# Optimization experiments

Hardware: AMD Instinct MI355X
Metric: run time of the kernel (lower is better)

The kernel has to match this reference:

```python
import jax, jax.numpy as jnp
import numpy as np

BATCH, N, DIM_IN, DIM_K, DIM_V, NH = 2, 4096, 256, 256, 256, 8

def setup_inputs() -> dict:
    key = jax.random.key(0)
    k1, k2, k3, k4 = jax.random.split(key, 4)
    s = 1.0 / np.sqrt(DIM_IN)
    return {
        "x": jax.random.normal(k1, (BATCH, N, DIM_IN), dtype=jnp.float32),
        "Wq": jax.random.normal(k2, (DIM_IN, DIM_K), dtype=jnp.float32) * s,
        "Wk": jax.random.normal(k3, (DIM_IN, DIM_K), dtype=jnp.float32) * s,
        "Wv": jax.random.normal(k4, (DIM_IN, DIM_V), dtype=jnp.float32) * s,
    }

def reference(x, Wq, Wk, Wv):
    b, n, _ = x.shape
    nh = NH
    dk = DIM_K // nh
    dv = DIM_V // nh
    # project and split heads: [b, nh, n, dk]
    q = jnp.einsum('bni,ik->bnk', x, Wq).reshape(b, n, nh, dk).transpose(0, 2, 1, 3)
    k = jnp.einsum('bni,ik->bnk', x, Wk).reshape(b, n, nh, dk).transpose(0, 2, 1, 3)
    v = jnp.einsum('bni,iv->bnv', x, Wv).reshape(b, n, nh, dv).transpose(0, 2, 1, 3)
    scale = 1.0 / np.sqrt(dk)
    dist = jnp.einsum('bhqd,bhkd->bhqk', q, k) * scale  # [b, nh, n, n]
    dist = jax.nn.softmax(dist, axis=-1)
    # dropout is identity in eval mode
    att = jnp.einsum('bhqk,bhkv->bhqv', dist, v)  # [b, nh, n, dv]
    return att.transpose(0, 2, 1, 3).reshape(b, n, DIM_V)
```

## Files before the change

kernel.cpp:

```cpp
#include <hip/hip_runtime.h>
#include <math.h>

#define BATCH 2
#define SEQ   4096
#define DIN   256
#define NH    8
#define DH    32
#define BH    (BATCH*NH)
#define NSPLIT 4
#define KRANGE (SEQ/NSPLIT)
#define TILES  (KRANGE/64)
#define QTILE  256

typedef short bf16x8 __attribute__((ext_vector_type(8)));
typedef float f32x4  __attribute__((ext_vector_type(4)));

#if defined(__has_builtin)
#if __has_builtin(__builtin_amdgcn_exp2f)
#define EXP2(x) __builtin_amdgcn_exp2f(x)
#else
#define EXP2_ASM 1
#endif
#else
#define EXP2_ASM 1
#endif
#ifdef EXP2_ASM
__device__ __forceinline__ float exp2_raw(float x) {
    float r;
    asm("v_exp_f32 %0, %1\n\ts_nop 1" : "=v"(r) : "v"(x));
    return r;
}
#define EXP2(x) exp2_raw(x)
#endif

#define SC2 0.25508218f

__device__ __forceinline__ unsigned short f2bf(float f) {
    unsigned int u = __builtin_bit_cast(unsigned int, f);
    u += 0x7fffu + ((u >> 16) & 1u);
    return (unsigned short)(u >> 16);
}

__device__ __forceinline__ unsigned int pack_bf2(float f0, float f1) {
    unsigned int u0 = __builtin_bit_cast(unsigned int, f0) + 0x8000u;
    unsigned int u1 = __builtin_bit_cast(unsigned int, f1) + 0x8000u;
    return __builtin_amdgcn_perm(u1, u0, 0x07060302u);
}

__device__ __forceinline__ unsigned int pack_bf2_t(float f0, float f1) {
    return __builtin_amdgcn_perm(__builtin_bit_cast(unsigned int, f1),
                                 __builtin_bit_cast(unsigned int, f0),
                                 0x07060302u);
}

#if defined(__has_builtin)
#if __has_builtin(__builtin_amdgcn_global_load_lds)
#define HAS_ASYNC_LDS 1
#endif
#endif

__device__ __forceinline__ void stage16(const unsigned short* g,
                                        unsigned short* lds_base, int lane) {
#ifdef HAS_ASYNC_LDS
    __builtin_amdgcn_global_load_lds(
        (const __attribute__((address_space(1))) unsigned int*)g,
        (__attribute__((address_space(3))) unsigned int*)lds_base, 16, 0, 0);
#else
    *(bf16x8*)(lds_base + (size_t)lane * 8) = *(const bf16x8*)g;
#endif
}

__global__ __launch_bounds__(256) void prep_kernel(
    const float* __restrict__ Wq, const float* __restrict__ Wk, const float* __restrict__ Wv,
    unsigned short* __restrict__ Wt)
{
    __shared__ float ws[64][65];
    const int t = threadIdx.x;
    int wsel = blockIdx.x >> 4;
    int tile = blockIdx.x & 15;
    int tr = (tile >> 2) * 64;
    int tc = (tile & 3) * 64;
    const float* __restrict__ W = (wsel == 0) ? Wq : (wsel == 1) ? Wk : Wv;
    #pragma unroll
    for (int i = 0; i < 16; i++) {
        int row = i * 4 + (t >> 6), col = t & 63;
        ws[row][col] = W[(size_t)(tr + row) * DIN + tc + col];
    }
    __syncthreads();
    unsigned short* dst = Wt + (size_t)wsel * DIN * DIN;
    #pragma unroll
    for (int i = 0; i < 16; i++) {
        int orow = i * 4 + (t >> 6), ocol = t & 63;
        dst[(size_t)(tc + orow) * DIN + tr + ocol] = f2bf(ws[ocol][orow]);
    }
}

__global__ __launch_bounds__(256) void proj_kernel(
    const float* __restrict__ x, const unsigned short* __restrict__ Wt,
    unsigned short* __restrict__ qh, unsigned short* __restrict__ kh,
    unsigned short* __restrict__ vt)
{
    __shared__ __align__(16) unsigned short abuf[8][4][64][8];
    __shared__ __align__(16) unsigned short bbuf[8][4][64][8];

    const int wsel = blockIdx.y;
    const int w    = threadIdx.x >> 6;
    const int lane = threadIdx.x & 63;
    const int quad = lane >> 4;
    const int l16  = lane & 15;

    const int sl   = lane ^ (lane >> 3);
    const int sl16 = sl >> 2, squad = sl & 3;
    const int s_ = (l16 << 2) | quad;
    const int jj = (s_ & 56) | ((s_ ^ (s_ >> 3)) & 7);

    int arow0, brow0;
    const unsigned short* Wbase;
    const float* Xbase;
    unsigned short (*wdst)[4][64][8];
    unsigned short (*xdst)[4][64][8];
    if (wsel < 2) {
        int tt = blockIdx.x >> 7, nt = blockIdx.x & 127;
        arow0 = tt * 64; brow0 = nt * 64;
        Wbase = Wt + (size_t)wsel * DIN * DIN + (size_t)arow0 * DIN;
        Xbase = x + (size_t)brow0 * DIN;
        wdst = abuf; xdst = bbuf;
    } else {
        int nt = blockIdx.x >> 2, tt = blockIdx.x & 3;
        arow0 = nt * 64; brow0 = tt * 64;
        Xbase = x + (size_t)arow0 * DIN;
        Wbase = Wt + (size_t)2 * DIN * DIN + (size_t)brow0 * DIN;
        wdst = bbuf; xdst = abuf;
    }

    #pragma unroll
    for (int i = 0; i < 8; i++) {
        int id = w * 8 + i;
        int kb = id >> 2, rt = id & 3;
        stage16(Wbase + (size_t)(rt * 16 + sl16) * DIN + kb * 32 + squad * 8,
                &wdst[kb][rt][0][0], lane);
    }
    #pragma unroll
    for (int i = 0; i < 8; i++) {
        int id = w * 8 + i;
        int kb = id >> 2, rt = id & 3;
        const float4* src = (const float4*)(Xbase + (size_t)(rt * 16 + sl16) * DIN
                                            + kb * 32 + squad * 8);
        float4 a = src[0], b = src[1];
        uint4 p = { pack_bf2(a.x, a.y), pack_bf2(a.z, a.w),
                    pack_bf2(b.x, b.y), pack_bf2(b.z, b.w) };
        *(uint4*)(&xdst[kb][rt][0][0] + (size_t)lane * 8) = p;
    }
    __syncthreads();

    f32x4 acc[4];
    #pragma unroll
    for (int c = 0; c < 4; c++) acc[c] = (f32x4){0.f, 0.f, 0.f, 0.f};
    #pragma unroll
    for (int kb = 0; kb < 8; kb++) {
        bf16x8 af = *(const bf16x8*)&abuf[kb][w][jj][0];
        #pragma unroll
        for (int c = 0; c < 4; c++) {
            bf16x8 bfr = *(const bf16x8*)&bbuf[kb][c][jj][0];
            acc[c] = __builtin_amdgcn_mfma_f32_16x16x32_bf16(af, bfr, acc[c], 0, 0, 0);
        }
    }

    if (wsel < 2) {
        const float scl = (wsel == 0) ? SC2 : 1.0f;
        unsigned short* __restrict__ dst0 = (wsel == 0) ? qh : kh;
        const int t0 = arow0 + w * 16;
        const int h = t0 >> 5, d0 = (t0 & 31) + quad * 4;
        #pragma unroll
        for (int c = 0; c < 4; c++) {
            int n = brow0 + c * 16 + l16;
            int b = n >> 12, n12 = n & 4095;
            unsigned int u01 = pack_bf2(acc[c][0] * scl, acc[c][1] * scl);
            unsigned int u23 = pack_bf2(acc[c][2] * scl, acc[c][3] * scl);
            *(uint2*)&dst0[((size_t)(b * NH + h) * SEQ + n12) * DH + d0] = make_uint2(u01, u23);
        }
    } else {
        const int n0w = arow0 + w * 16;
        const int b = n0w >> 12, nbase = (n0w & 4095) + quad * 4;
        #pragma unroll
        for (int c = 0; c < 4; c++) {
            int t = brow0 + c * 16;
            int h = t >> 5, d = (t & 31) + l16;
            unsigned int u01 = pack_bf2(acc[c][0], acc[c][1]);
            unsigned int u23 = pack_bf2(acc[c][2], acc[c][3]);
            *(uint2*)&vt[((size_t)(b * NH + h) * DH + d) * SEQ + nbase] = make_uint2(u01, u23);
        }
    }
}

__global__ __launch_bounds__(256, 4) void attn_kernel(
    const unsigned short* __restrict__ qh,
    const unsigned short* __restrict__ kh,
    const unsigned short* __restrict__ vt,
    unsigned short* __restrict__ po, float* __restrict__ pl)
{
    __shared__ __align__(16) unsigned short pbuf[4][2][16][64];
    __shared__ __align__(16) unsigned short kbuf[2][4][64][8];
    __shared__ __align__(16) unsigned short vbuf[2][4][64][8];

    const int tid  = threadIdx.x;
    const int wave = tid >> 6;
    const int lane = tid & 63;
    const int quad = lane >> 4;
    const int l16  = lane & 15;
    const int sw   = l16 & 7;

    const int bh = blockIdx.x & 15;
    const int qb = (blockIdx.x >> 4) & 15;
    const int ks = blockIdx.x >> 8;
    const int q0 = qb * QTILE + wave * 64;
    const int kbase = ks * KRANGE;

    const unsigned short* __restrict__ Qp = qh + (size_t)bh * SEQ * DH;
    const unsigned short* __restrict__ Kp = kh + (size_t)bh * SEQ * DH;
    const unsigned short* __restrict__ Vp = vt + (size_t)bh * DH * SEQ;

    const int sl    = lane ^ (lane >> 3);
    const int sl16  = sl >> 2, squad = sl & 3;
    const unsigned short* ksrc = Kp + (size_t)(kbase + wave * 16 + sl16) * DH + squad * 8;
    const int vdh = wave >> 1, vkh = wave & 1;
    const unsigned short* vsrc = Vp + (size_t)(vdh * 16 + sl16) * SEQ + kbase + vkh * 32 + squad * 8;

    const int s_ = (l16 << 2) | quad;
    const int jj = (s_ & 56) | ((s_ ^ (s_ >> 3)) & 7);

    bf16x8 qf[4];
    #pragma unroll
    for (int i = 0; i < 4; i++)
        qf[i] = *(const bf16x8*)(Qp + (size_t)(q0 + i * 16 + l16) * DH + quad * 8);

    const bf16x8 ones = {0x3F80, 0x3F80, 0x3F80, 0x3F80,
                         0x3F80, 0x3F80, 0x3F80, 0x3F80};

    f32x4 o[4][2];
    f32x4 lones[4];
    #pragma unroll
    for (int i = 0; i < 4; i++) {
        o[i][0] = (f32x4){0.f, 0.f, 0.f, 0.f};
        o[i][1] = (f32x4){0.f, 0.f, 0.f, 0.f};
        lones[i] = (f32x4){0.f, 0.f, 0.f, 0.f};
    }
    const f32x4 z = {0.f, 0.f, 0.f, 0.f};

    stage16(ksrc, &kbuf[0][wave][0][0], lane);
    stage16(vsrc, &vbuf[0][wave][0][0], lane);
    ksrc += 64 * DH;
    vsrc += 64;

    for (int t = 0; t < TILES; t++) {
        const int buf = t & 1;

        __syncthreads();

        if (t + 1 < TILES) {
            stage16(ksrc, &kbuf[buf ^ 1][wave][0][0], lane);
            stage16(vsrc, &vbuf[buf ^ 1][wave][0][0], lane);
            ksrc += 64 * DH;
            vsrc += 64;
        }

        bf16x8 kf[4], vf[4];
        #pragma unroll
        for (int c = 0; c < 4; c++) kf[c] = *(const bf16x8*)&kbuf[buf][c][jj][0];
        #pragma unroll
        for (int f = 0; f < 4; f++) vf[f] = *(const bf16x8*)&vbuf[buf][f][jj][0];

        #pragma unroll
        for (int qt = 0; qt < 4; qt++) {
            const int pr = qt & 1;
            #pragma unroll
            for (int c = 0; c < 4; c++) {
                f32x4 s = __builtin_amdgcn_mfma_f32_16x16x32_bf16(kf[c], qf[qt], z, 0, 0, 0);
                float e0 = EXP2(s[0]);
                float e1 = EXP2(s[1]);
                float e2 = EXP2(s[2]);
                float e3 = EXP2(s[3]);
                int chs = ((c * 2 + (quad >> 1)) ^ sw) * 8 + (quad & 1) * 4;
                *(uint2*)&pbuf[wave][pr][l16][chs] =
                    make_uint2(pack_bf2_t(e0, e1), pack_bf2_t(e2, e3));
            }
            bf16x8 pf0 = *(const bf16x8*)&pbuf[wave][pr][l16][((0 + quad) ^ sw) * 8];
            bf16x8 pf1 = *(const bf16x8*)&pbuf[wave][pr][l16][((4 + quad) ^ sw) * 8];
            __builtin_amdgcn_s_setprio(1);
            o[qt][0] = __builtin_amdgcn_mfma_f32_16x16x32_bf16(pf0, vf[0], o[qt][0], 0, 0, 0);
            o[qt][0] = __builtin_amdgcn_mfma_f32_16x16x32_bf16(pf1, vf[1], o[qt][0], 0, 0, 0);
            o[qt][1] = __builtin_amdgcn_mfma_f32_16x16x32_bf16(pf0, vf[2], o[qt][1], 0, 0, 0);
            o[qt][1] = __builtin_amdgcn_mfma_f32_16x16x32_bf16(pf1, vf[3], o[qt][1], 0, 0, 0);
            lones[qt] = __builtin_amdgcn_mfma_f32_16x16x32_bf16(pf0, ones, lones[qt], 0, 0, 0);
            lones[qt] = __builtin_amdgcn_mfma_f32_16x16x32_bf16(pf1, ones, lones[qt], 0, 0, 0);
            __builtin_amdgcn_s_setprio(0);
        }
    }

    const size_t obase = (size_t)(ks * BH + bh) * SEQ;
    #pragma unroll
    for (int qt = 0; qt < 4; qt++) {
        if (l16 == 0) {
            #pragma unroll
            for (int r = 0; r < 4; r++)
                pl[obase + q0 + qt * 16 + quad * 4 + r] = lones[qt][r];
        }
        #pragma unroll
        for (int r = 0; r < 4; r++) {
            int n = q0 + qt * 16 + quad * 4 + r;
            unsigned short* dst = po + (obase + n) * DH;
            dst[l16]      = f2bf(o[qt][0][r]);
            dst[16 + l16] = f2bf(o[qt][1][r]);
        }
    }
}

__global__ __launch_bounds__(256) void merge_kernel(
    const unsigned short* __restrict__ po, const float* __restrict__ pl,
    float* __restrict__ out)
{
    int t    = blockIdx.x * 256 + threadIdx.x;
    int d8   = t & 7;
    int pair = t >> 3;
    int bh   = pair >> 12;
    int n    = pair & 4095;
    float s0 = 0.f, s1 = 0.f, s2 = 0.f, s3 = 0.f, ls = 0.f;
    #pragma unroll
    for (int sp = 0; sp < NSPLIT; sp++) {
        size_t base = (size_t)(sp * BH + bh) * SEQ + n;
        uint2 v = ((const uint2*)(po + base * DH))[d8];
        s0 += __builtin_bit_cast(float, v.x << 16);
        s1 += __builtin_bit_cast(float, v.x & 0xFFFF0000u);
        s2 += __builtin_bit_cast(float, v.y << 16);
        s3 += __builtin_bit_cast(float, v.y & 0xFFFF0000u);
        ls += pl[base];
    }
    float inv = 1.f / ls;
    int b = bh >> 3, h = bh & 7;
    float4 o = {s0 * inv, s1 * inv, s2 * inv, s3 * inv};
    ((float4*)(out + ((size_t)b * SEQ + n) * (NH * DH) + h * DH))[d8] = o;
}

extern "C" void kernel_launch(void* const* d_in, const int* in_sizes, int n_in,
                              void* d_out, int out_size, void* d_ws, size_t ws_size,
                              hipStream_t stream)
{
    const float* x  = (const float*)d_in[0];
    const float* Wq = (const float*)d_in[1];
    const float* Wk = (const float*)d_in[2];
    const float* Wv = (const float*)d_in[3];
    float* out = (float*)d_out;

    unsigned short* qh = (unsigned short*)d_ws;
    unsigned short* kh = qh + (size_t)BH * SEQ * DH;
    unsigned short* vt = kh + (size_t)BH * SEQ * DH;
    unsigned short* Wt = vt + (size_t)BH * SEQ * DH;
    unsigned short* po = Wt + 3 * DIN * DIN;
    float* pl = (float*)(po + (size_t)NSPLIT * BH * SEQ * DH);

    prep_kernel<<<dim3(48), 256, 0, stream>>>(Wq, Wk, Wv, Wt);
    proj_kernel<<<dim3(512, 3), 256, 0, stream>>>(x, Wt, qh, kh, vt);
    attn_kernel<<<dim3(BH * (SEQ / QTILE) * NSPLIT), 256, 0, stream>>>(qh, kh, vt, po, pl);
    merge_kernel<<<dim3(2048), 256, 0, stream>>>(po, pl, out);
}
```

Measured before the change: 134.5 us.

## Replace LDS P-transpose with permlane swaps and software-pipeline QK/PV steps

Rebuilds the softmax probability fragments for the PV MFMA with permlane32/permlane16 swap instructions instead of writing to and reading back from a shared-memory buffer. This removes the LDS round trip and its waits. The per-tile loop is also manually pipelined so the QK MFMA for the next query tile is issued before the PV MFMAs of the previous one, and the whole section runs at raised priority. Launch bounds drop from 4 to 3 waves per SIMD, which gives more registers at the cost of occupancy; the old LDS path is kept as a fallback when the builtins are missing.

```diff
diff --git a/kernel.cpp b/kernel.cpp
--- a/kernel.cpp
+++ b/kernel.cpp
@@ -31,6 +31,12 @@
     return r;
 }
 #define EXP2(x) exp2_raw(x)
+#endif
+
+#if defined(__has_builtin)
+#if __has_builtin(__builtin_amdgcn_permlane32_swap) && __has_builtin(__builtin_amdgcn_permlane16_swap)
+#define HAS_PERMSWAP 1
+#endif
 #endif
 
 #define SC2 0.25508218f
@@ -193,13 +199,50 @@
     }
 }
 
-__global__ __launch_bounds__(256, 4) void attn_kernel(
+#define QK_STEP(qt, S)                                                        \
+    { _Pragma("unroll")                                                       \
+      for (int c_ = 0; c_ < 4; c_++)                                          \
+          S[c_] = __builtin_amdgcn_mfma_f32_16x16x32_bf16(kf[c_], qf[qt], z, 0, 0, 0); }
+
+#define SM_STEP(S, W)                                                         \
+    { _Pragma("unroll")                                                       \
+      for (int c_ = 0; c_ < 4; c_++) {                                        \
+          W[c_][0] = pack_bf2_t(EXP2(S[c_][0]), EXP2(S[c_][1]));              \
+          W[c_][1] = pack_bf2_t(EXP2(S[c_][2]), EXP2(S[c_][3]));              \
+      } }
+
+#define PERM_STEP(W, P0, P1)                                                  \
+    { u32x2 a_, b_; uint4 f0_, f1_;                                           \
+      a_ = __builtin_amdgcn_permlane32_swap(W[0][0], W[1][0], false, false);  \
+      b_ = __builtin_amdgcn_permlane16_swap(a_.x, a_.y, false, false);        \
+      f0_.x = b_.x; f0_.z = b_.y;                                             \
+      a_ = __builtin_amdgcn_permlane32_swap(W[0][1], W[1][1], false, false);  \
+      b_ = __builtin_amdgcn_permlane16_swap(a_.x, a_.y, false, false);        \
+      f0_.y = b_.x; f0_.w = b_.y;                                             \
+      a_ = __builtin_amdgcn_permlane32_swap(W[2][0], W[3][0], false, false);  \
+      b_ = __builtin_amdgcn_permlane16_swap(a_.x, a_.y, false, false);        \
+      f1_.x = b_.x; f1_.z = b_.y;                                             \
+      a_ = __builtin_amdgcn_permlane32_swap(W[2][1], W[3][1], false, false);  \
+      b_ = __builtin_amdgcn_permlane16_swap(a_.x, a_.y, false, false);        \
+      f1_.y = b_.x; f1_.w = b_.y;                                             \
+      P0 = __builtin_bit_cast(bf16x8, f0_);                                   \
+      P1 = __builtin_bit_cast(bf16x8, f1_); }
+
+#define PV_STEP(P0, P1, qt)                                                   \
+    { o[qt][0] = __builtin_amdgcn_mfma_f32_16x16x32_bf16(P0, vf[0], o[qt][0], 0, 0, 0); \
+      o[qt][0] = __builtin_amdgcn_mfma_f32_16x16x32_bf16(P1, vf[1], o[qt][0], 0, 0, 0); \
+      o[qt][1] = __builtin_amdgcn_mfma_f32_16x16x32_bf16(P0, vf[2], o[qt][1], 0, 0, 0); \
+      o[qt][1] = __builtin_amdgcn_mfma_f32_16x16x32_bf16(P1, vf[3], o[qt][1], 0, 0, 0); \
+      lones[qt] = __builtin_amdgcn_mfma_f32_16x16x32_bf16(P0, ones, lones[qt], 0, 0, 0); \
+      lones[qt] = __builtin_amdgcn_mfma_f32_16x16x32_bf16(P1, ones, lones[qt], 0, 0, 0); }
+
+__global__ __launch_bounds__(256, 3) void attn_kernel(
     const unsigned short* __restrict__ qh,
     const unsigned short* __restrict__ kh,
     const unsigned short* __restrict__ vt,
     unsigned short* __restrict__ po, float* __restrict__ pl)
 {
-    __shared__ __align__(16) unsigned short pbuf[4][2][16][64];
+    typedef unsigned int u32x2 __attribute__((ext_vector_type(2)));
     __shared__ __align__(16) unsigned short kbuf[2][4][64][8];
     __shared__ __align__(16) unsigned short vbuf[2][4][64][8];
 
@@ -208,7 +251,6 @@
     const int lane = tid & 63;
     const int quad = lane >> 4;
     const int l16  = lane & 15;
-    const int sw   = l16 & 7;
 
     const int bh = blockIdx.x & 15;
     const int qb = (blockIdx.x >> 4) & 15;
@@ -270,31 +312,37 @@
         #pragma unroll
         for (int f = 0; f < 4; f++) vf[f] = *(const bf16x8*)&vbuf[buf][f][jj][0];
 
+#ifdef HAS_PERMSWAP
+        f32x4 S[4];
+        unsigned int W[4][2];
+        bf16x8 p0, p1;
+
+        __builtin_amdgcn_s_setprio(1);
+        QK_STEP(0, S); SM_STEP(S, W); PERM_STEP(W, p0, p1);
+        QK_STEP(1, S); PV_STEP(p0, p1, 0); SM_STEP(S, W); PERM_STEP(W, p0, p1);
+        QK_STEP(2, S); PV_STEP(p0, p1, 1); SM_STEP(S, W); PERM_STEP(W, p0, p1);
+        QK_STEP(3, S); PV_STEP(p0, p1, 2); SM_STEP(S, W); PERM_STEP(W, p0, p1);
+        PV_STEP(p0, p1, 3);
+        __builtin_amdgcn_s_setprio(0);
+#else
+        __shared__ __align__(16) unsigned short pbuf[4][2][16][64];
+        const int sw = l16 & 7;
         #pragma unroll
         for (int qt = 0; qt < 4; qt++) {
             const int pr = qt & 1;
             #pragma unroll
             for (int c = 0; c < 4; c++) {
                 f32x4 s = __builtin_amdgcn_mfma_f32_16x16x32_bf16(kf[c], qf[qt], z, 0, 0, 0);
-                float e0 = EXP2(s[0]);
-                float e1 = EXP2(s[1]);
-                float e2 = EXP2(s[2]);
-                float e3 = EXP2(s[3]);
                 int chs = ((c * 2 + (quad >> 1)) ^ sw) * 8 + (quad & 1) * 4;
                 *(uint2*)&pbuf[wave][pr][l16][chs] =
-                    make_uint2(pack_bf2_t(e0, e1), pack_bf2_t(e2, e3));
+                    make_uint2(pack_bf2_t(EXP2(s[0]), EXP2(s[1])),
+                               pack_bf2_t(EXP2(s[2]), EXP2(s[3])));
             }
             bf16x8 pf0 = *(const bf16x8*)&pbuf[wave][pr][l16][((0 + quad) ^ sw) * 8];
             bf16x8 pf1 = *(const bf16x8*)&pbuf[wave][pr][l16][((4 + quad) ^ sw) * 8];
-            __builtin_amdgcn_s_setprio(1);
-            o[qt][0] = __builtin_amdgcn_mfma_f32_16x16x32_bf16(pf0, vf[0], o[qt][0], 0, 0, 0);
-            o[qt][0] = __builtin_amdgcn_mfma_f32_16x16x32_bf16(pf1, vf[1], o[qt][0], 0, 0, 0);
-            o[qt][1] = __builtin_amdgcn_mfma_f32_16x16x32_bf16(pf0, vf[2], o[qt][1], 0, 0, 0);
-            o[qt][1] = __builtin_amdgcn_mfma_f32_16x16x32_bf16(pf1, vf[3], o[qt][1], 0, 0, 0);
-            lones[qt] = __builtin_amdgcn_mfma_f32_16x16x32_bf16(pf0, ones, lones[qt], 0, 0, 0);
-            lones[qt] = __builtin_amdgcn_mfma_f32_16x16x32_bf16(pf1, ones, lones[qt], 0, 0, 0);
-            __builtin_amdgcn_s_setprio(0);
-        }
+            PV_STEP(pf0, pf1, qt);
+        }
+#endif
     }
 
     const size_t obase = (size_t)(ks * BH + bh) * SEQ;
```

New measurement: 148.0 us. 1.1x slower.
